# Kernel tuning notes

Measured on AMD Instinct MI355X. Metric: run time of the kernel, lower is better.

## Reference

```python
import jax, jax.numpy as jnp
import numpy as np

N, K, M, DIN, DOUT = 4096, 16, 65536, 256, 256


def setup_inputs() -> dict:
    key = jax.random.key(0)
    ks = jax.random.split(key, 16)
    s = 1.0 / np.sqrt(DOUT)
    x = jax.random.normal(ks[0], (N, DIN), jnp.float32)
    h_tensor = jax.random.normal(ks[1], (M, DOUT), jnp.float32)
    c_tensor = jax.random.normal(ks[2], (M, DOUT), jnp.float32)
    # variable-length child lists: lengths in [1, K], -1 padding like get_nums()
    lengths = jax.random.randint(ks[3], (N,), 1, K + 1)
    idx = jax.random.randint(ks[4], (N, K), 0, M)
    t = jnp.arange(K)[None, :]
    indice = jnp.where(t < lengths[:, None], idx, -1).astype(jnp.int32)
    W_w = jax.random.normal(ks[5], (4 * DOUT, DIN), jnp.float32) * s
    W_b = jax.random.normal(ks[6], (4 * DOUT,), jnp.float32) * s
    h0 = jax.random.normal(ks[7], (4, DOUT), jnp.float32)
    c0 = jax.random.normal(ks[8], (4, DOUT), jnp.float32)
    Wih = jax.random.normal(ks[9], (4, 2, 4 * DOUT, DOUT), jnp.float32) * s
    Whh = jax.random.normal(ks[10], (4, 2, 4 * DOUT, DOUT), jnp.float32) * s
    bih = jax.random.normal(ks[11], (4, 2, 4 * DOUT), jnp.float32) * s
    bhh = jax.random.normal(ks[12], (4, 2, 4 * DOUT), jnp.float32) * s
    fc = jax.random.normal(ks[13], (4, DOUT, 2 * DOUT), jnp.float32) * s
    return dict(x=x, h_tensor=h_tensor, c_tensor=c_tensor, indice=indice,
                W_w=W_w, W_b=W_b, h0=h0, c0=c0, Wih=Wih, Whh=Whh,
                bih=bih, bhh=bhh, fc=fc)


def _lstm_dir(xseq, mask, h_init, c_init, W_ih, W_hh, b, reverse):
    """Masked LSTM over child axis. xseq [N,K,d], mask [N,K] bool. Mimics
    pack_padded_sequence: state frozen and output 0 at padded steps."""
    d = h_init.shape[-1]
    xs = jnp.swapaxes(xseq, 0, 1)   # [K,N,d]
    ms = jnp.swapaxes(mask, 0, 1)   # [K,N]

    def step(carry, inp):
        h, c = carry
        xt, mt = inp
        g = xt @ W_ih.T + h @ W_hh.T + b        # [N,4d], gate order i,f,g,o
        i = jax.nn.sigmoid(g[:, :d])
        f = jax.nn.sigmoid(g[:, d:2 * d])
        u = jnp.tanh(g[:, 2 * d:3 * d])
        o = jax.nn.sigmoid(g[:, 3 * d:])
        c_new = f * c + i * u
        h_new = o * jnp.tanh(c_new)
        m = mt[:, None]
        return (jnp.where(m, h_new, h), jnp.where(m, c_new, c)), jnp.where(m, h_new, 0.0)

    _, ys = jax.lax.scan(step, (h_init, c_init), (xs, ms), reverse=reverse)
    return jnp.swapaxes(ys, 0, 1)   # [N,K,d]


def _bilstm_seq(xseq, mask, h0j, c0j, Wihj, Whhj, bihj, bhhj, fcj):
    n = xseq.shape[0]
    h_init = jnp.broadcast_to(h0j, (n, h0j.shape[-1]))
    c_init = jnp.broadcast_to(c0j, (n, c0j.shape[-1]))
    yf = _lstm_dir(xseq, mask, h_init, c_init, Wihj[0], Whhj[0], bihj[0] + bhhj[0], False)
    yb = _lstm_dir(xseq, mask, h_init, c_init, Wihj[1], Whhj[1], bihj[1] + bhhj[1], True)
    y = jnp.concatenate([yf, yb], axis=-1)      # [N,K,2d]
    return jnp.einsum('nkh,dh->nkd', y, fcj)    # fc (no bias); 0 stays 0 at pads


def reference(x, h_tensor, c_tensor, indice, W_w, W_b, h0, c0, Wih, Whh, bih, bhh, fc):
    mask = indice != -1                           # [N,K]
    length = mask.sum(axis=1)                     # [N], >= 1
    safe_idx = jnp.where(mask, indice, 0)
    h = h_tensor[safe_idx]                        # [N,K,d] gather of child states
    c = c_tensor[safe_idx]
    Wx = x @ W_w.T + W_b                          # [N,4d]
    d = DOUT
    Wf, Wi, Wu, Wo = Wx[:, :d], Wx[:, d:2 * d], Wx[:, 2 * d:3 * d], Wx[:, 3 * d:]
    ys = [_bilstm_seq(h, mask, h0[j], c0[j], Wih[j], Whh[j], bih[j], bhh[j], fc[j])
          for j in range(4)]                      # U_f, U_i, U_u, U_o
    # forget branch: per-child gate, masked sum over children
    branch_f_k = jax.nn.sigmoid(Wf[:, None, :] + ys[0])
    branch_f = jnp.sum(branch_f_k * c * mask[..., None], axis=1)
    # i/u/o use last valid timestep (packed LSTM y_last)
    ar = jnp.arange(x.shape[0])
    last = length - 1
    branch_i = jax.nn.sigmoid(ys[1][ar, last] + Wi)
    branch_u = jnp.tanh(ys[2][ar, last] + Wu)
    branch_o = jax.nn.sigmoid(ys[3][ar, last] + Wo)
    new_c = branch_i * branch_u + branch_f
    new_h = branch_o * jnp.tanh(new_c)
    return new_h, new_c
```

## Files before the change

kernel.cpp:

```cpp
#include <hip/hip_runtime.h>
#include <math.h>

#define N_SEQ 4096
#define KCH   16
#define DM    256
#define G4    1024
#define LP    40
#define EP    68

typedef __attribute__((ext_vector_type(8))) short bf8;
typedef __attribute__((ext_vector_type(4))) float f4;

__device__ __forceinline__ float fast_rcp(float x) { return __builtin_amdgcn_rcpf(x); }
__device__ __forceinline__ float sigf(float x)   { return fast_rcp(1.f + __expf(-x)); }
__device__ __forceinline__ float tanh_f(float x) { return 1.f - 2.f * fast_rcp(1.f + __expf(2.f * x)); }

__device__ __forceinline__ float bf2f(unsigned short u) {
    return __uint_as_float(((unsigned)u) << 16);
}
__device__ __forceinline__ unsigned short f2bf(float f) {
    unsigned u = __float_as_uint(f);
    unsigned r = (u + 0x7fffu + ((u >> 16) & 1u)) >> 16;
    return (unsigned short)r;
}
__device__ __forceinline__ unsigned pack2(float a, float b) {
    return (unsigned)f2bf(a) | ((unsigned)f2bf(b) << 16);
}

#define GLDS(gp, lp) __builtin_amdgcn_global_load_lds( \
    (const __attribute__((address_space(1))) void*)(gp), \
    (__attribute__((address_space(3))) void*)(lp), 16, 0, 0)

template<int KLEN, int LDB>
__device__ __forceinline__ void pass_glk(
    const unsigned short* __restrict__ a0,
    const unsigned short* __restrict__ b0,
    unsigned short* Asm, unsigned short* Bsm,
    unsigned short* la0, unsigned short* lb0,
    f4 (&acc)[4][4], int wm, int wn, int jq, int fr)
{
    const unsigned short* a1 = a0 + 16 * DM;
    const unsigned short* b1 = b0 + 16 * LDB;
#pragma unroll
    for (int k0 = 0; k0 < KLEN; k0 += 32) {
        __syncthreads();
        GLDS(a0 + k0, la0);
        GLDS(a1 + k0, la0 + 512);
        GLDS(b0 + k0, lb0);
        GLDS(b1 + k0, lb0 + 512);
        __syncthreads();
        bf8 af[4], bb[4];
#pragma unroll
        for (int i = 0; i < 4; ++i)
            af[i] = *(const bf8*)(Asm + (wm + i * 16 + fr) * 32 + jq);
#pragma unroll
        for (int j = 0; j < 4; ++j)
            bb[j] = *(const bf8*)(Bsm + (wn + j * 16 + fr) * 32 + jq);
#pragma unroll
        for (int i = 0; i < 4; ++i)
#pragma unroll
            for (int j = 0; j < 4; ++j)
                acc[i][j] = __builtin_amdgcn_mfma_f32_16x16x32_bf16(
                    af[i], bb[j], acc[i][j], 0, 0, 0);
    }
}

template<int KLEN>
__device__ __forceinline__ void pass_bf(
    const unsigned short* __restrict__ aRow,
    const unsigned short* __restrict__ bRow,
    unsigned short* Asm, unsigned short* Bsm, f4 (&acc)[4][4])
{
    const int tid  = threadIdx.x;
    const int kh   = (tid & 1) * 16;
    const int srow = tid >> 1;
    const int lane = tid & 63, wave = tid >> 6;
    const int wm = (wave >> 1) * 64, wn = (wave & 1) * 64;
    const int fr = lane & 15, fk = (lane >> 4) * 8;
    unsigned short* da = Asm + srow * LP + kh;
    unsigned short* db = Bsm + srow * LP + kh;

    for (int k0 = 0; k0 < KLEN; k0 += 32) {
        __syncthreads();
        *(int4*)(da)     = *(const int4*)(aRow + k0 + kh);
        *(int4*)(da + 8) = *(const int4*)(aRow + k0 + kh + 8);
        *(int4*)(db)     = *(const int4*)(bRow + k0 + kh);
        *(int4*)(db + 8) = *(const int4*)(bRow + k0 + kh + 8);
        __syncthreads();
        bf8 af[4], bb[4];
#pragma unroll
        for (int i = 0; i < 4; ++i)
            af[i] = *(const bf8*)(Asm + (wm + i * 16 + fr) * LP + fk);
#pragma unroll
        for (int j = 0; j < 4; ++j)
            bb[j] = *(const bf8*)(Bsm + (wn + j * 16 + fr) * LP + fk);
#pragma unroll
        for (int i = 0; i < 4; ++i)
#pragma unroll
            for (int j = 0; j < 4; ++j)
                acc[i][j] = __builtin_amdgcn_mfma_f32_16x16x32_bf16(
                    af[i], bb[j], acc[i][j], 0, 0, 0);
    }
}

template<int KLEN>
__device__ __forceinline__ void pass_f32(
    const float* __restrict__ aRow,
    const unsigned short* __restrict__ bRow,
    unsigned short* Asm, unsigned short* Bsm, f4 (&acc)[4][4])
{
    const int tid  = threadIdx.x;
    const int kh   = (tid & 1) * 16;
    const int srow = tid >> 1;
    const int lane = tid & 63, wave = tid >> 6;
    const int wm = (wave >> 1) * 64, wn = (wave & 1) * 64;
    const int fr = lane & 15, fk = (lane >> 4) * 8;
    unsigned short* da = Asm + srow * LP + kh;
    unsigned short* db = Bsm + srow * LP + kh;

    for (int k0 = 0; k0 < KLEN; k0 += 32) {
        __syncthreads();
        {
            const float* s = aRow + k0 + kh;
            float4 v0 = *(const float4*)(s);
            float4 v1 = *(const float4*)(s + 4);
            float4 v2 = *(const float4*)(s + 8);
            float4 v3 = *(const float4*)(s + 12);
            *(int4*)(da)     = make_int4(pack2(v0.x, v0.y), pack2(v0.z, v0.w),
                                         pack2(v1.x, v1.y), pack2(v1.z, v1.w));
            *(int4*)(da + 8) = make_int4(pack2(v2.x, v2.y), pack2(v2.z, v2.w),
                                         pack2(v3.x, v3.y), pack2(v3.z, v3.w));
        }
        *(int4*)(db)     = *(const int4*)(bRow + k0 + kh);
        *(int4*)(db + 8) = *(const int4*)(bRow + k0 + kh + 8);
        __syncthreads();
        bf8 af[4], bb[4];
#pragma unroll
        for (int i = 0; i < 4; ++i)
            af[i] = *(const bf8*)(Asm + (wm + i * 16 + fr) * LP + fk);
#pragma unroll
        for (int j = 0; j < 4; ++j)
            bb[j] = *(const bf8*)(Bsm + (wn + j * 16 + fr) * LP + fk);
#pragma unroll
        for (int i = 0; i < 4; ++i)
#pragma unroll
            for (int j = 0; j < 4; ++j)
                acc[i][j] = __builtin_amdgcn_mfma_f32_16x16x32_bf16(
                    af[i], bb[j], acc[i][j], 0, 0, 0);
    }
}


__global__ __launch_bounds__(256) void k_lastidx(
    const int* __restrict__ indice, int* __restrict__ last_idx)
{
    const int n = blockIdx.x * 256 + threadIdx.x;
    if (n >= N_SEQ) return;
    int len = 0;
#pragma unroll
    for (int k = 0; k < KCH; ++k) len += (indice[n * KCH + k] != -1);
    last_idx[n] = indice[n * KCH + (len - 1)];
}

__global__ __launch_bounds__(1024) void k_hh0_bsum2(
    const float* __restrict__ bih, const float* __restrict__ bhh,
    const float* __restrict__ h0, const float* __restrict__ Whh,
    float* __restrict__ bsum2)
{
    const int jz = blockIdx.x, j = jz + 1;
    const int g = threadIdx.x;
    const int jd = j * 2 + 1;
    const float* wrow = Whh + ((size_t)jd * G4 + g) * DM;
    float s = bih[jd * G4 + g] + bhh[jd * G4 + g];
    for (int h = 0; h < DM; ++h) s = fmaf(h0[j * DM + h], wrow[h], s);
    const int c = (g & 255) * 4 + (g >> 8);
    bsum2[jz * G4 + c] = s;
}

__global__ __launch_bounds__(256) void k_init_states(
    const float* __restrict__ h0, const float* __restrict__ c0,
    unsigned short* __restrict__ hA, float* __restrict__ c_state)
{
    const int row = blockIdx.x;
    const int s = row >> 12;
    const int tree = (s < 4) ? s : 0;
    const int d = threadIdx.x;
    hA[(size_t)row * DM + d]      = f2bf(h0[tree * DM + d]);
    c_state[(size_t)row * DM + d] = c0[tree * DM + d];
}

__global__ __launch_bounds__(256) void k_zero4(float4* __restrict__ p)
{
    p[(size_t)blockIdx.x * 256 + threadIdx.x] = make_float4(0.f, 0.f, 0.f, 0.f);
}

__global__ __launch_bounds__(256) void k_prep_wcat(
    const float* __restrict__ Wih, const float* __restrict__ Whh,
    const float* __restrict__ bih, const float* __restrict__ bhh,
    unsigned short* __restrict__ wcat, float* __restrict__ bsumr)
{
    const int c = blockIdx.x, s = blockIdx.y;
    const int wsel = (s < 4) ? s * 2 : 1;
    const int d = c >> 2, g = c & 3;
    const size_t srcrow = ((size_t)wsel * G4 + g * DM + d) * DM;
    unsigned short* dst = wcat + ((size_t)s * G4 + c) * 512;
    const int t = threadIdx.x;
    dst[t]       = f2bf(Wih[srcrow + t]);
    dst[256 + t] = f2bf(Whh[srcrow + t]);
    if (t == 0)
        bsumr[s * G4 + c] = bih[wsel * G4 + g * DM + d] + bhh[wsel * G4 + g * DM + d];
}

__global__ __launch_bounds__(256) void k_prep_wcat2(
    const float* __restrict__ Wih, unsigned short* __restrict__ wcat2)
{
    const int c = blockIdx.x, jz = blockIdx.y, j = jz + 1;
    const int d = c >> 2, g = c & 3;
    const size_t srcrow = ((size_t)(j * 2 + 1) * G4 + g * DM + d) * DM;
    wcat2[((size_t)jz * G4 + c) * 256 + threadIdx.x] = f2bf(Wih[srcrow + threadIdx.x]);
}

__global__ __launch_bounds__(256) void k_prep_fcb(
    const float* __restrict__ fc, unsigned short* __restrict__ fcb)
{
    const int dout = blockIdx.x, z = blockIdx.y, t = threadIdx.x;
    fcb[((size_t)z * DM + dout) * DM + t] = f2bf(fc[(size_t)dout * 512 + z * DM + t]);
}

__global__ __launch_bounds__(256) void k_prep_fcb2(
    const float* __restrict__ fc, unsigned short* __restrict__ fcb2)
{
    const int dout = blockIdx.x, jz = blockIdx.y, j = jz + 1, t = threadIdx.x;
    const float* src = fc + ((size_t)j * DM + dout) * 512;
    unsigned short* dst = fcb2 + ((size_t)jz * DM + dout) * 512;
    dst[t]       = f2bf(src[t]);
    dst[t + 256] = f2bf(src[t + 256]);
}

__global__ __launch_bounds__(256) void k_prep_wwb(
    const float* __restrict__ W_w, unsigned short* __restrict__ wwb)
{
    const size_t i = (size_t)blockIdx.x * 256 + threadIdx.x;
    wwb[i] = f2bf(W_w[i]);
}

__device__ __forceinline__ void gather_slice(
    const float* __restrict__ h_tensor, const int* __restrict__ indice,
    unsigned short* __restrict__ xbuf, int zz, int kk, int blk)
{
    const int row = blk * 64 + (threadIdx.x >> 2);
    const int cb  = (threadIdx.x & 3) * 64;
    int idx = indice[row * KCH + kk]; if (idx < 0) idx = 0;
    const float* src = h_tensor + (size_t)idx * DM + cb;
    unsigned short* dst = xbuf + ((size_t)zz * N_SEQ + row) * DM + cb;
#pragma unroll
    for (int c = 0; c < 64; c += 4) {
        float4 v = *(const float4*)(src + c);
        *(uint2*)(dst + c) = make_uint2(pack2(v.x, v.y), pack2(v.z, v.w));
    }
}

__global__ __launch_bounds__(256) void k_gather_x0(
    const float* __restrict__ h_tensor, const int* __restrict__ indice,
    unsigned short* __restrict__ xbuf)
{
    const int slice = blockIdx.x >> 6, blk = blockIdx.x & 63;
    gather_slice(h_tensor, indice, xbuf, slice, slice ? (KCH - 1) : 0, blk);
}

__global__ __launch_bounds__(256) void k_scan_merged(
    const unsigned short* __restrict__ xb_cur, unsigned short* __restrict__ xb_nxt,
    const unsigned short* __restrict__ yb_prev, unsigned short* __restrict__ yb_cur,
    const int* __restrict__ indice, const float* __restrict__ h_tensor,
    const unsigned short* __restrict__ h_in, unsigned short* __restrict__ h_out,
    float* __restrict__ c_state,
    const unsigned short* __restrict__ wcat, const float* __restrict__ bsumr,
    const unsigned short* __restrict__ fcb, unsigned short* __restrict__ ys0,
    int r)
{
    __shared__ __align__(16) unsigned short SMEM[8704];
    unsigned short* Asm = SMEM;
    unsigned short* Bsm = SMEM + 4096;

    const int tid  = threadIdx.x;
    const int lane = tid & 63, wave = tid >> 6;
    const int wm = (wave >> 1) * 64, wn = (wave & 1) * 64;
    const int fr = lane & 15;
    const int jq = ((lane >> 4) ^ ((fr >> 1) & 3)) * 8;
    const int lr = wave * 32 + (lane >> 2);
    const int jl = ((lane & 3) ^ ((lane >> 3) & 3)) * 8;
    unsigned short* la0 = Asm + wave * 1024;
    unsigned short* lb0 = Bsm + wave * 1024;

    const int bz = blockIdx.z;

    if (bz == 5) {
        const int id5 = blockIdx.x + 8 * blockIdx.y;
        if (id5 >= 128) {
            const int rr = r + 1;
            if (rr >= KCH) return;
            const int g = id5 - 128;
            const int zz = g >> 6;
            gather_slice(h_tensor, indice, xb_nxt, zz,
                         zz ? (KCH - 1 - rr) : rr, g & 63);
            return;
        }
        if (r == 0) return;
        const int rp = r - 1;
        const int z = id5 >> 6;
        const int kslice = z ? (KCH - 1 - rp) : rp;
        const int row0 = (id5 & 31) * 128;
        const int c0 = ((id5 >> 5) & 1) * 128;

        const unsigned short* ay0 = yb_prev + ((size_t)z * N_SEQ + row0 + lr) * DM + jl;
        const unsigned short* bf0 = fcb + ((size_t)z * DM + c0 + lr) * DM + jl;

        f4 acc[4][4];
#pragma unroll
        for (int i = 0; i < 4; ++i)
#pragma unroll
            for (int j = 0; j < 4; ++j) acc[i][j] = (f4)(0.f);
        pass_glk<256, 256>(ay0, bf0, Asm, Bsm, la0, lb0, acc, wm, wn, jq, fr);

#pragma unroll
        for (int i = 0; i < 4; ++i)
#pragma unroll
            for (int j = 0; j < 4; ++j) {
                const int col = c0 + wn + j * 16 + fr;
#pragma unroll
                for (int reg = 0; reg < 4; ++reg) {
                    const int rowg = row0 + wm + i * 16 + (lane >> 4) * 4 + reg;
                    const size_t ix = ((size_t)rowg * KCH + kslice) * DM + col;
                    ys0[ix] = f2bf(bf2f(ys0[ix]) + acc[i][j][reg]);
                }
            }
        return;
    }

    const int s = bz;
    const int k = (s < 4) ? r : (KCH - 1 - r);
    const int z = (s < 4) ? 0 : 1;
    const int bn = blockIdx.y & 7;
    const int bm = (blockIdx.y >> 3) * 8 + blockIdx.x;
    const int row0 = bm * 128, c0 = bn * 128;

    const unsigned short* xz = xb_cur + (size_t)z * N_SEQ * DM;
    const unsigned short* hs_in = h_in + (size_t)s * N_SEQ * DM;
    const unsigned short* ax0 = xz + (size_t)(row0 + lr) * DM + jl;
    const unsigned short* ah0 = hs_in + (size_t)(row0 + lr) * DM + jl;
    const unsigned short* bw0 = wcat + ((size_t)s * G4 + c0 + lr) * 512 + jl;

    f4 acc[4][4];
#pragma unroll
    for (int i = 0; i < 4; ++i)
#pragma unroll
        for (int j = 0; j < 4; ++j) acc[i][j] = (f4)(0.f);

    pass_glk<256, 512>(ax0, bw0, Asm, Bsm, la0, lb0, acc, wm, wn, jq, fr);
    pass_glk<256, 512>(ah0, bw0 + 256, Asm, Bsm, la0, lb0, acc, wm, wn, jq, fr);

    float* sc = (float*)SMEM + wave * (16 * EP);
    __syncthreads();
#pragma unroll
    for (int i = 0; i < 4; ++i) {
#pragma unroll
        for (int j = 0; j < 4; ++j) {
            const int colL = j * 16 + fr;
            const int rbase = (lane >> 4) * 4;
#pragma unroll
            for (int reg = 0; reg < 4; ++reg)
                sc[(rbase + reg) * EP + colL] = acc[i][j][reg];
        }
        __syncthreads();
        const int rowg = row0 + wm + i * 16 + fr;
        const bool m = (indice[rowg * KCH + k] != -1);
#pragma unroll
        for (int q = 0; q < 4; ++q) {
            const int dL = (lane >> 4) + q * 4;
            const f4 gv = *(const f4*)(sc + fr * EP + dL * 4);
            const f4 bb = *(const f4*)(bsumr + s * G4 + c0 + wn + dL * 4);
            const int d = ((c0 + wn) >> 2) + dL;
            const float ii = sigf(gv.x + bb.x);
            const float ff = sigf(gv.y + bb.y);
            const float uu = tanh_f(gv.z + bb.z);
            const float oo = sigf(gv.w + bb.w);
            const size_t cix = ((size_t)s * N_SEQ + rowg) * DM + d;
            const float c_old = c_state[cix];
            const float cn = ff * c_old + ii * uu;
            const float cw = m ? cn : c_old;
            c_state[cix] = cw;
            const float hn = oo * tanh_f(cn);
            const unsigned short hv = m ? f2bf(hn) : hs_in[(size_t)rowg * DM + d];
            h_out[cix] = hv;
            if (s == 0)
                yb_cur[(size_t)rowg * DM + d] = m ? f2bf(hn) : (unsigned short)0;
            else if (s == 4)
                yb_cur[(size_t)(N_SEQ + rowg) * DM + d] = m ? f2bf(hn) : (unsigned short)0;
        }
        __syncthreads();
    }
}

__global__ __launch_bounds__(256) void k_acc_tail(
    const unsigned short* __restrict__ ybuf, const unsigned short* __restrict__ fcb,
    unsigned short* __restrict__ ys0)
{
    __shared__ __align__(16) unsigned short SMEM[8192];
    unsigned short* Asm = SMEM;
    unsigned short* Bsm = SMEM + 4096;
    const int tid = threadIdx.x;
    const int lane = tid & 63, wave = tid >> 6;
    const int wm = (wave >> 1) * 64, wn = (wave & 1) * 64;
    const int fr = lane & 15;
    const int jq = ((lane >> 4) ^ ((fr >> 1) & 3)) * 8;
    const int lr = wave * 32 + (lane >> 2);
    const int jl = ((lane & 3) ^ ((lane >> 3) & 3)) * 8;
    unsigned short* la0 = Asm + wave * 1024;
    unsigned short* lb0 = Bsm + wave * 1024;

    const int z = blockIdx.z;
    const int kslice = z ? 0 : (KCH - 1);
    const int row0 = blockIdx.y * 128, c0 = blockIdx.x * 128;

    const unsigned short* ay0 = ybuf + ((size_t)z * N_SEQ + row0 + lr) * DM + jl;
    const unsigned short* bf0 = fcb + ((size_t)z * DM + c0 + lr) * DM + jl;

    f4 acc[4][4];
#pragma unroll
    for (int i = 0; i < 4; ++i)
#pragma unroll
        for (int j = 0; j < 4; ++j) acc[i][j] = (f4)(0.f);
    pass_glk<256, 256>(ay0, bf0, Asm, Bsm, la0, lb0, acc, wm, wn, jq, fr);

#pragma unroll
    for (int i = 0; i < 4; ++i)
#pragma unroll
        for (int j = 0; j < 4; ++j) {
            const int col = c0 + wn + j * 16 + fr;
#pragma unroll
            for (int reg = 0; reg < 4; ++reg) {
                const int rowg = row0 + wm + i * 16 + (lane >> 4) * 4 + reg;
                const size_t ix = ((size_t)rowg * KCH + kslice) * DM + col;
                ys0[ix] = f2bf(bf2f(ys0[ix]) + acc[i][j][reg]);
            }
        }
}


__global__ __launch_bounds__(256) void k_bwd_mfma(
    const float* __restrict__ h_tensor, const int* __restrict__ last_idx,
    const unsigned short* __restrict__ wcat2, const float* __restrict__ bsum2,
    const float* __restrict__ c0, unsigned short* __restrict__ yb_last)
{
    __shared__ __align__(16) unsigned short SMEM[2 * 128 * LP];
    const int jz = blockIdx.z, j = jz + 1;
    const int row0 = blockIdx.y * 128, c0t = blockIdx.x * 128;
    const int tid = threadIdx.x;
    const int srow = tid >> 1;

    const float* aF = h_tensor + (size_t)last_idx[row0 + srow] * DM;
    const unsigned short* bR = wcat2 + ((size_t)jz * G4 + c0t + srow) * 256;

    f4 acc[4][4];
#pragma unroll
    for (int i = 0; i < 4; ++i)
#pragma unroll
        for (int jj = 0; jj < 4; ++jj) acc[i][jj] = (f4)(0.f);

    pass_f32<256>(aF, bR, SMEM, SMEM + 128 * LP, acc);

    const int lane = tid & 63, wave = tid >> 6;
    const int wm = (wave >> 1) * 64, wn = (wave & 1) * 64;
    float* sc = (float*)SMEM + wave * (16 * EP);

    __syncthreads();
#pragma unroll
    for (int i = 0; i < 4; ++i) {
#pragma unroll
        for (int jj = 0; jj < 4; ++jj) {
            const int colL = jj * 16 + (lane & 15);
            const int rbase = (lane >> 4) * 4;
#pragma unroll
            for (int reg = 0; reg < 4; ++reg)
                sc[(rbase + reg) * EP + colL] = acc[i][jj][reg];
        }
        __syncthreads();
        const int rowg = row0 + wm + i * 16 + (lane & 15);
#pragma unroll
        for (int q = 0; q < 4; ++q) {
            const int dL = (lane >> 4) + q * 4;
            const f4 gv = *(const f4*)(sc + (lane & 15) * EP + dL * 4);
            const f4 bb = *(const f4*)(bsum2 + jz * G4 + c0t + wn + dL * 4);
            const int d = ((c0t + wn) >> 2) + dL;
            const float ii = sigf(gv.x + bb.x);
            const float ff = sigf(gv.y + bb.y);
            const float uu = tanh_f(gv.z + bb.z);
            const float oo = sigf(gv.w + bb.w);
            const float cn = ff * c0[j * DM + d] + ii * uu;
            yb_last[((size_t)jz * N_SEQ + rowg) * DM + d] = f2bf(oo * tanh_f(cn));
        }
        __syncthreads();
    }
}

__global__ __launch_bounds__(256) void k_wx_mfma(
    const float* __restrict__ x, const unsigned short* __restrict__ wwb,
    const float* __restrict__ W_b, unsigned short* __restrict__ Wx)
{
    __shared__ __align__(16) unsigned short SMEM[2 * 128 * LP];
    const int row0 = blockIdx.y * 128, c0 = blockIdx.x * 128;
    const int tid = threadIdx.x;
    const int srow = tid >> 1;

    const float* aF = x + (size_t)(row0 + srow) * DM;
    const unsigned short* bR = wwb + (size_t)(c0 + srow) * DM;

    f4 acc[4][4];
#pragma unroll
    for (int i = 0; i < 4; ++i)
#pragma unroll
        for (int j = 0; j < 4; ++j) acc[i][j] = (f4)(0.f);

    pass_f32<256>(aF, bR, SMEM, SMEM + 128 * LP, acc);

    const int lane = tid & 63, wave = tid >> 6;
    const int wm = (wave >> 1) * 64, wn = (wave & 1) * 64;
#pragma unroll
    for (int i = 0; i < 4; ++i)
#pragma unroll
        for (int j = 0; j < 4; ++j) {
            const int col = c0 + wn + j * 16 + (lane & 15);
            const float bv = W_b[col];
#pragma unroll
            for (int reg = 0; reg < 4; ++reg) {
                const int rowg = row0 + wm + i * 16 + (lane >> 4) * 4 + reg;
                Wx[(size_t)rowg * G4 + col] = f2bf(acc[i][j][reg] + bv);
            }
        }
}

__global__ __launch_bounds__(256) void k_fc_last_mfma(
    const unsigned short* __restrict__ h_final, const unsigned short* __restrict__ yb_last,
    const unsigned short* __restrict__ fcb2, unsigned short* __restrict__ ys_last)
{
    __shared__ __align__(16) unsigned short SMEM[2 * 128 * LP];
    const int jz = blockIdx.z;
    const int row0 = blockIdx.y * 128, c0 = blockIdx.x * 128;
    const int tid = threadIdx.x;
    const int srow = tid >> 1;

    const unsigned short* aH1 = h_final + ((size_t)(1 + jz) * N_SEQ + row0 + srow) * DM;
    const unsigned short* aH2 = yb_last + ((size_t)jz * N_SEQ + row0 + srow) * DM;
    const unsigned short* bR  = fcb2 + ((size_t)jz * DM + c0 + srow) * 512;

    f4 acc[4][4];
#pragma unroll
    for (int i = 0; i < 4; ++i)
#pragma unroll
        for (int j = 0; j < 4; ++j) acc[i][j] = (f4)(0.f);

    pass_bf<256>(aH1, bR, SMEM, SMEM + 128 * LP, acc);
    pass_bf<256>(aH2, bR + 256, SMEM, SMEM + 128 * LP, acc);

    const int lane = tid & 63, wave = tid >> 6;
    const int wm = (wave >> 1) * 64, wn = (wave & 1) * 64;
#pragma unroll
    for (int i = 0; i < 4; ++i)
#pragma unroll
        for (int j = 0; j < 4; ++j) {
            const int col = c0 + wn + j * 16 + (lane & 15);
#pragma unroll
            for (int reg = 0; reg < 4; ++reg) {
                const int rowg = row0 + wm + i * 16 + (lane >> 4) * 4 + reg;
                ys_last[((size_t)jz * N_SEQ + rowg) * DM + col] = f2bf(acc[i][j][reg]);
            }
        }
}

__global__ __launch_bounds__(256) void k_final(
    const unsigned short* __restrict__ Wx, const unsigned short* __restrict__ ys0,
    const unsigned short* __restrict__ ys_last, const float* __restrict__ c_tensor,
    const int* __restrict__ indice, float* __restrict__ out)
{
    const int n = blockIdx.x, d = threadIdx.x;
    const float Wf = bf2f(Wx[(size_t)n * G4 + d]);
    const float Wi = bf2f(Wx[(size_t)n * G4 + DM + d]);
    const float Wu = bf2f(Wx[(size_t)n * G4 + 2 * DM + d]);
    const float Wo = bf2f(Wx[(size_t)n * G4 + 3 * DM + d]);
    float bf = 0.f;
#pragma unroll
    for (int k = 0; k < KCH; ++k) {
        const int id = indice[n * KCH + k];
        if (id >= 0)
            bf += sigf(Wf + bf2f(ys0[((size_t)n * KCH + k) * DM + d])) *
                  c_tensor[(size_t)id * DM + d];
    }
    const float bi = sigf(bf2f(ys_last[((size_t)0 * N_SEQ + n) * DM + d]) + Wi);
    const float bu = tanh_f(bf2f(ys_last[((size_t)1 * N_SEQ + n) * DM + d]) + Wu);
    const float bo = sigf(bf2f(ys_last[((size_t)2 * N_SEQ + n) * DM + d]) + Wo);
    const float nc = bi * bu + bf;
    const float nh = bo * tanh_f(nc);
    out[(size_t)n * DM + d] = nh;
    out[(size_t)N_SEQ * DM + (size_t)n * DM + d] = nc;
}

extern "C" void kernel_launch(void* const* d_in, const int* in_sizes, int n_in,
                              void* d_out, int out_size, void* d_ws, size_t ws_size,
                              hipStream_t stream)
{
    const float* x        = (const float*)d_in[0];
    const float* h_tensor = (const float*)d_in[1];
    const float* c_tensor = (const float*)d_in[2];
    const int*   indice   = (const int*)d_in[3];
    const float* W_w      = (const float*)d_in[4];
    const float* W_b      = (const float*)d_in[5];
    const float* h0       = (const float*)d_in[6];
    const float* c0       = (const float*)d_in[7];
    const float* Wih      = (const float*)d_in[8];
    const float* Whh      = (const float*)d_in[9];
    const float* bih      = (const float*)d_in[10];
    const float* bhh      = (const float*)d_in[11];
    const float* fc       = (const float*)d_in[12];
    float* out = (float*)d_out;

    char* base = (char*)d_ws;
    float*          c_state  = (float*)(base + 0);
    int*            last_idx = (int*)  (base + 20971520);
    float*          bsumr    = (float*)(base + 20987904);
    unsigned short* hA       = (unsigned short*)(base + 21008384);
    unsigned short* hB       = (unsigned short*)(base + 31494144);
    unsigned short* ys0      = (unsigned short*)(base + 41979904);
    unsigned short* ybufA    = (unsigned short*)(base + 75534336);
    unsigned short* ybufB    = (unsigned short*)(base + 79728640);
    unsigned short* xbufA    = (unsigned short*)(base + 83922944);
    unsigned short* fcb      = (unsigned short*)(base + 88117248);
    unsigned short* postbuf  = (unsigned short*)(base + 88379392);
    unsigned short* wcat     = (unsigned short*)(base + 92573696);
    const size_t need = 97816576;
    if (ws_size < need) return;

    unsigned short* xbufB   = postbuf;
    unsigned short* wcat2   = postbuf;
    unsigned short* fcb2    = postbuf + 786432;
    unsigned short* wwb     = postbuf + 1179648;
    float*          bsum2   = (float*)(postbuf + 1441792);
    unsigned short* yb_last = ybufA;
    unsigned short* ys_last = hB;
    unsigned short* WxBuf   = hA;

    k_lastidx<<<16, 256, 0, stream>>>(indice, last_idx);
    k_init_states<<<5 * N_SEQ, 256, 0, stream>>>(h0, c0, hA, c_state);
    k_zero4<<<8192, 256, 0, stream>>>((float4*)ys0);
    k_prep_wcat<<<dim3(G4, 5), 256, 0, stream>>>(Wih, Whh, bih, bhh, wcat, bsumr);
    k_prep_fcb<<<dim3(DM, 2), 256, 0, stream>>>(fc, fcb);
    k_gather_x0<<<128, 256, 0, stream>>>(h_tensor, indice, xbufA);

    for (int r = 0; r < KCH; ++r) {
        const unsigned short* xb_cur = (r & 1) ? xbufB : xbufA;
        unsigned short* xb_nxt       = (r & 1) ? xbufA : xbufB;
        const unsigned short* yb_prev = (r & 1) ? ybufA : ybufB;
        unsigned short* yb_cur        = (r & 1) ? ybufB : ybufA;
        const unsigned short* h_in = (r & 1) ? hB : hA;
        unsigned short* h_out      = (r & 1) ? hA : hB;
        k_scan_merged<<<dim3(8, 32, 6), 256, 0, stream>>>(
            xb_cur, xb_nxt, yb_prev, yb_cur, indice, h_tensor,
            h_in, h_out, c_state, wcat, bsumr, fcb, ys0, r);
    }

    k_acc_tail<<<dim3(2, 32, 2), 256, 0, stream>>>(ybufB, fcb, ys0);

    k_prep_wcat2<<<dim3(G4, 3), 256, 0, stream>>>(Wih, wcat2);
    k_hh0_bsum2<<<3, 1024, 0, stream>>>(bih, bhh, h0, Whh, bsum2);
    k_prep_fcb2<<<dim3(DM, 3), 256, 0, stream>>>(fc, fcb2);
    k_prep_wwb<<<1024, 256, 0, stream>>>(W_w, wwb);

    k_bwd_mfma<<<dim3(8, 32, 3), 256, 0, stream>>>(
        h_tensor, last_idx, wcat2, bsum2, c0, yb_last);
    k_fc_last_mfma<<<dim3(2, 32, 3), 256, 0, stream>>>(hA, yb_last, fcb2, ys_last);
    k_wx_mfma<<<dim3(8, 32), 256, 0, stream>>>(x, wwb, W_b, WxBuf);

    k_final<<<N_SEQ, 256, 0, stream>>>(WxBuf, ys0, ys_last, c_tensor, indice, out);
}
```

Before: 1.505 ms.

## Double-buffer LDS tiles in MFMA GEMM passes to overlap loads with compute

Replaces the single-buffered global-to-LDS load loop with a two-stage ping-pong pipeline. The next K-slice is prefetched with global_load_lds while MFMAs run on the current slice, and explicit vmcnt waits plus raw s_barrier replace the full __syncthreads pairs. The x and h passes are merged into one segmented loop so the pipeline carries across them. Shared memory per block doubles to 32KB, which may reduce occupancy. Correctness depends on the hand-written waitcnt counts.

```diff
diff --git a/kernel.cpp b/kernel.cpp
--- a/kernel.cpp
+++ b/kernel.cpp
@@ -31,37 +31,55 @@
     (const __attribute__((address_space(1))) void*)(gp), \
     (__attribute__((address_space(3))) void*)(lp), 16, 0, 0)
 
-template<int KLEN, int LDB>
-__device__ __forceinline__ void pass_glk(
-    const unsigned short* __restrict__ a0,
-    const unsigned short* __restrict__ b0,
-    unsigned short* Asm, unsigned short* Bsm,
-    unsigned short* la0, unsigned short* lb0,
-    f4 (&acc)[4][4], int wm, int wn, int jq, int fr)
-{
-    const unsigned short* a1 = a0 + 16 * DM;
-    const unsigned short* b1 = b0 + 16 * LDB;
-#pragma unroll
-    for (int k0 = 0; k0 < KLEN; k0 += 32) {
-        __syncthreads();
-        GLDS(a0 + k0, la0);
-        GLDS(a1 + k0, la0 + 512);
-        GLDS(b0 + k0, lb0);
-        GLDS(b1 + k0, lb0 + 512);
-        __syncthreads();
+template<int NSEG, int LDB>
+__device__ __forceinline__ void pass_pipe(
+    const unsigned short* const (&segA)[NSEG],
+    const unsigned short* const (&segB)[NSEG],
+    unsigned short* SM,
+    f4 (&acc)[4][4], int wave, int wm, int wn, int jq, int fr)
+{
+    unsigned short* const la[2] = { SM + wave * 1024,        SM + 8192 + wave * 1024 };
+    unsigned short* const lb[2] = { SM + 4096 + wave * 1024, SM + 12288 + wave * 1024 };
+    constexpr int NS = NSEG * 8;
+
+    {
+        const unsigned short* A_ = segA[0];
+        const unsigned short* B_ = segB[0];
+        GLDS(A_, la[0]);             GLDS(A_ + 16 * DM, la[0] + 512);
+        GLDS(B_, lb[0]);             GLDS(B_ + 16 * LDB, lb[0] + 512);
+    }
+#pragma unroll
+    for (int t = 0; t < NS; ++t) {
+        if (t + 1 < NS) {
+            const unsigned short* A_ = segA[(t + 1) >> 3] + ((t + 1) & 7) * 32;
+            const unsigned short* B_ = segB[(t + 1) >> 3] + ((t + 1) & 7) * 32;
+            const int nb = (t + 1) & 1;
+            GLDS(A_, la[nb]);        GLDS(A_ + 16 * DM, la[nb] + 512);
+            GLDS(B_, lb[nb]);        GLDS(B_ + 16 * LDB, lb[nb] + 512);
+            asm volatile("s_waitcnt vmcnt(4)" ::: "memory");
+        } else {
+            asm volatile("s_waitcnt vmcnt(0)" ::: "memory");
+        }
+        __builtin_amdgcn_s_barrier();
+
+        const unsigned short* Ab = SM + (t & 1) * 8192;
+        const unsigned short* Bb = Ab + 4096;
         bf8 af[4], bb[4];
 #pragma unroll
         for (int i = 0; i < 4; ++i)
-            af[i] = *(const bf8*)(Asm + (wm + i * 16 + fr) * 32 + jq);
+            af[i] = *(const bf8*)(Ab + (wm + i * 16 + fr) * 32 + jq);
 #pragma unroll
         for (int j = 0; j < 4; ++j)
-            bb[j] = *(const bf8*)(Bsm + (wn + j * 16 + fr) * 32 + jq);
+            bb[j] = *(const bf8*)(Bb + (wn + j * 16 + fr) * 32 + jq);
 #pragma unroll
         for (int i = 0; i < 4; ++i)
 #pragma unroll
             for (int j = 0; j < 4; ++j)
                 acc[i][j] = __builtin_amdgcn_mfma_f32_16x16x32_bf16(
                     af[i], bb[j], acc[i][j], 0, 0, 0);
+
+        asm volatile("s_waitcnt lgkmcnt(0)" ::: "memory");
+        __builtin_amdgcn_s_barrier();
     }
 }
 
@@ -278,9 +296,7 @@
     const unsigned short* __restrict__ fcb, unsigned short* __restrict__ ys0,
     int r)
 {
-    __shared__ __align__(16) unsigned short SMEM[8704];
-    unsigned short* Asm = SMEM;
-    unsigned short* Bsm = SMEM + 4096;
+    __shared__ __align__(16) unsigned short SMEM[16384];
 
     const int tid  = threadIdx.x;
     const int lane = tid & 63, wave = tid >> 6;
@@ -289,8 +305,6 @@
     const int jq = ((lane >> 4) ^ ((fr >> 1) & 3)) * 8;
     const int lr = wave * 32 + (lane >> 2);
     const int jl = ((lane & 3) ^ ((lane >> 3) & 3)) * 8;
-    unsigned short* la0 = Asm + wave * 1024;
-    unsigned short* lb0 = Bsm + wave * 1024;
 
     const int bz = blockIdx.z;
 
@@ -320,7 +334,11 @@
         for (int i = 0; i < 4; ++i)
 #pragma unroll
             for (int j = 0; j < 4; ++j) acc[i][j] = (f4)(0.f);
-        pass_glk<256, 256>(ay0, bf0, Asm, Bsm, la0, lb0, acc, wm, wn, jq, fr);
+        {
+            const unsigned short* const segA[1] = { ay0 };
+            const unsigned short* const segB[1] = { bf0 };
+            pass_pipe<1, 256>(segA, segB, SMEM, acc, wave, wm, wn, jq, fr);
+        }
 
 #pragma unroll
         for (int i = 0; i < 4; ++i)
@@ -356,8 +374,11 @@
 #pragma unroll
         for (int j = 0; j < 4; ++j) acc[i][j] = (f4)(0.f);
 
-    pass_glk<256, 512>(ax0, bw0, Asm, Bsm, la0, lb0, acc, wm, wn, jq, fr);
-    pass_glk<256, 512>(ah0, bw0 + 256, Asm, Bsm, la0, lb0, acc, wm, wn, jq, fr);
+    {
+        const unsigned short* const segA[2] = { ax0, ah0 };
+        const unsigned short* const segB[2] = { bw0, bw0 + 256 };
+        pass_pipe<2, 512>(segA, segB, SMEM, acc, wave, wm, wn, jq, fr);
+    }
 
     float* sc = (float*)SMEM + wave * (16 * EP);
     __syncthreads();
@@ -405,9 +426,7 @@
     const unsigned short* __restrict__ ybuf, const unsigned short* __restrict__ fcb,
     unsigned short* __restrict__ ys0)
 {
-    __shared__ __align__(16) unsigned short SMEM[8192];
-    unsigned short* Asm = SMEM;
-    unsigned short* Bsm = SMEM + 4096;
+    __shared__ __align__(16) unsigned short SMEM[16384];
     const int tid = threadIdx.x;
     const int lane = tid & 63, wave = tid >> 6;
     const int wm = (wave >> 1) * 64, wn = (wave & 1) * 64;
@@ -415,8 +434,6 @@
     const int jq = ((lane >> 4) ^ ((fr >> 1) & 3)) * 8;
     const int lr = wave * 32 + (lane >> 2);
     const int jl = ((lane & 3) ^ ((lane >> 3) & 3)) * 8;
-    unsigned short* la0 = Asm + wave * 1024;
-    unsigned short* lb0 = Bsm + wave * 1024;
 
     const int z = blockIdx.z;
     const int kslice = z ? 0 : (KCH - 1);
@@ -430,7 +447,11 @@
     for (int i = 0; i < 4; ++i)
 #pragma unroll
         for (int j = 0; j < 4; ++j) acc[i][j] = (f4)(0.f);
-    pass_glk<256, 256>(ay0, bf0, Asm, Bsm, la0, lb0, acc, wm, wn, jq, fr);
+    {
+        const unsigned short* const segA[1] = { ay0 };
+        const unsigned short* const segB[1] = { bf0 };
+        pass_pipe<1, 256>(segA, segB, SMEM, acc, wave, wm, wn, jq, fr);
+    }
 
 #pragma unroll
     for (int i = 0; i < 4; ++i)
```

After: 1.390 ms. 1.08x faster.
